# Kernel tuning notes

Measured on AMD Instinct MI355X. Metric: run time of the kernel, lower is better.

## Reference

```python
import jax, jax.numpy as jnp
import numpy as np
import math

B, L, D = 8, 2048, 768
ORDER, EMB = 128, 5
FFT = 2 * L
MIN_DECAY = math.log(0.01) / 1.5   # slow_decay_pct = 1.5
MAX_DECAY = math.log(0.01) / 0.3   # fast_decay_pct = 0.3
SHIFT = 0.0


def _pos_emb(seq_len, emb_dim):
    # pos_emb_init from the source: [t, Re(z), Im(z)] with bands = (emb_dim-1)//2
    bands = (emb_dim - 1) // 2
    t = jnp.linspace(0.0, 1.0, seq_len)[None, :, None]
    t_res = jnp.linspace(0.0, seq_len - 1, seq_len)[None, :, None]
    w = 2.0 * jnp.pi * t_res / seq_len
    f = jnp.linspace(1e-4, bands - 1, bands)[None, None]
    zc = jnp.exp(-1j * f * w)
    return jnp.concatenate([t, zc.real, zc.imag], axis=-1).astype(jnp.float32)  # (1, L, EMB)


def setup_inputs() -> dict:
    key = jax.random.key(0)
    ks = jax.random.split(key, 16)
    s = 0.02
    return {
        "u": jax.random.normal(ks[0], (B, L, D), jnp.float32),
        "in_W": jax.random.normal(ks[1], (D, 3 * D), jnp.float32) * s,
        "in_b": jnp.zeros((3 * D,), jnp.float32),
        "out_W": jax.random.normal(ks[2], (D, D), jnp.float32) * s,
        "out_b": jnp.zeros((D,), jnp.float32),
        "x1_s": jax.random.normal(ks[3], (D, 4), jnp.float32) * 0.25,
        "x2_s": jax.random.normal(ks[4], (D, 4), jnp.float32) * 0.25,
        "v_s": jax.random.normal(ks[5], (D, 4), jnp.float32) * 0.25,
        "x1_sb": jax.random.normal(ks[6], (D,), jnp.float32) * 0.1,
        "x2_sb": jax.random.normal(ks[7], (D,), jnp.float32) * 0.1,
        "v_sb": jax.random.normal(ks[8], (D,), jnp.float32) * 0.1,
        "D_bias": jax.random.normal(ks[9], (D,), jnp.float32),
        "z": _pos_emb(L, EMB),
        "sin_freq": 10.0 * jnp.ones((1, ORDER), jnp.float32),   # hyena_w = 10
        "eo_mat": jax.random.normal(ks[10], (1, EMB, ORDER), jnp.float32) * 0.3,
        "eo_bias": jnp.zeros((1, ORDER), jnp.float32),
        "oo1_mat": jax.random.normal(ks[11], (1, ORDER, ORDER), jnp.float32) * 0.08,
        "oo1_bias": jnp.zeros((1, ORDER), jnp.float32),
        "oo2_mat": jax.random.normal(ks[12], (1, ORDER, ORDER), jnp.float32) * 0.08,
        "oo2_bias": jnp.zeros((1, ORDER), jnp.float32),
        "oh_mat": jax.random.normal(ks[13], (1, ORDER, D), jnp.float32) * 0.08,
    }


def _depthwise4(x, w, b):
    # torch Conv1d(groups=3D, kernel=4, padding=3) truncated to [:L] == causal conv, left pad 3
    out = jax.lax.conv_general_dilated(
        x, w[:, None, :], window_strides=(1,), padding=[(3, 0)],
        dimension_numbers=("NCH", "OIH", "NCH"), feature_group_count=x.shape[1])
    return out + b[None, :, None]


def _hyena_filter(z, sin_freq, eo_mat, eo_bias, oo1_mat, oo1_bias, oo2_mat, oo2_bias, oh_mat):
    # then exponential decay modulation (exp_mod_in_place_fwd), channels=1, reverse=0.
    f = sin_freq[:, None, :]                                       # (1, 1, ORDER)
    h = jnp.sin(f * (jnp.einsum("cle,ceo->clo", z, eo_mat) + eo_bias[:, None, :]))
    h = jnp.sin(f * (jnp.einsum("clo,cop->clp", h, oo1_mat) + oo1_bias[:, None, :]))
    h = jnp.sin(f * (jnp.einsum("clo,cop->clp", h, oo2_mat) + oo2_bias[:, None, :]))
    k = jnp.einsum("clo,coh->clh", h, oh_mat)                      # (1, L, D)
    t = jnp.linspace(0.0, 1.0, k.shape[1])
    deltas = jnp.abs(jnp.linspace(MIN_DECAY, MAX_DECAY, k.shape[2]))
    k = k * (jnp.exp(-t[None, :, None] * deltas[None, None, :]) + SHIFT)
    return k[0].T                                                  # (D, L)


def _forward(u, in_W, in_b, out_W, out_b, x1_s, x2_s, v_s, x1_sb, x2_sb, v_sb,
             D_bias, z, sin_freq, eo_mat, eo_bias, oo1_mat, oo1_bias,
             oo2_mat, oo2_bias, oh_mat):
    seqlen = u.shape[1]
    k = _hyena_filter(z, sin_freq, eo_mat, eo_bias, oo1_mat, oo1_bias, oo2_mat, oo2_bias, oh_mat)
    x1x2v = u @ in_W + in_b                                        # (B, L, 3D)
    x1, x2, v = jnp.split(x1x2v, 3, axis=-1)
    x1 = jnp.transpose(x1, (0, 2, 1))                              # (B, D, L)
    x2 = jnp.transpose(x2, (0, 2, 1))
    v = jnp.transpose(v, (0, 2, 1))
    x1 = _depthwise4(x1, x1_s, x1_sb)
    x2 = _depthwise4(x2, x2_s, x2_sb)
    v = _depthwise4(v, v_s, v_sb)
    v = v * x1                                                     # first gate
    k_f = jnp.fft.rfft(k.astype(jnp.float32), n=FFT)               # (D, FFT//2+1)
    v_f = jnp.fft.rfft(v.astype(jnp.float32), n=FFT)               # (B, D, FFT//2+1)
    y = jnp.fft.irfft(v_f * k_f[None], n=FFT)[..., :seqlen]        # long FFT conv
    y = y + v * D_bias[None, :, None]                              # skip term
    y = y * x2                                                     # second gate
    y = jnp.transpose(y, (0, 2, 1))                                # (B, L, D)
    return y @ out_W + out_b


def reference(u, in_W, in_b, out_W, out_b, x1_s, x2_s, v_s, x1_sb, x2_sb, v_sb,
              D_bias, z, sin_freq, eo_mat, eo_bias, oo1_mat, oo1_bias,
              oo2_mat, oo2_bias, oh_mat):
    return _forward(u, in_W, in_b, out_W, out_b, x1_s, x2_s, v_s, x1_sb, x2_sb, v_sb,
                    D_bias, z, sin_freq, eo_mat, eo_bias, oo1_mat, oo1_bias,
                    oo2_mat, oo2_bias, oh_mat)
```

## Files before the change

kernel.cpp:

```cpp
#include <hip/hip_runtime.h>


typedef __bf16 bf16x8 __attribute__((ext_vector_type(8)));
typedef float  f32x4  __attribute__((ext_vector_type(4)));

#define AS1 __attribute__((address_space(1)))
#define AS3 __attribute__((address_space(3)))
#define GLD16(gp, lp) __builtin_amdgcn_global_load_lds((AS1 void*)(void*)(gp), (AS3 void*)(void*)(lp), 16, 0, 0)

#define LGKM_BAR       __asm__ __volatile__("s_waitcnt lgkmcnt(0)\n\ts_barrier" ::: "memory")
#define VM_LGKM_BAR(N) __asm__ __volatile__("s_waitcnt vmcnt(" #N ") lgkmcnt(0)\n\ts_barrier" ::: "memory")

__device__ __forceinline__ unsigned short f2b(float f) {
    unsigned u = __builtin_bit_cast(unsigned, f);
    unsigned r = (u + 0x7fffu + ((u >> 16) & 1u)) >> 16;
    return (unsigned short)r;
}
__device__ __forceinline__ float b2f_lo(unsigned u) {
    return __builtin_bit_cast(float, u << 16);
}
__device__ __forceinline__ float b2f_hi(unsigned u) {
    return __builtin_bit_cast(float, u & 0xffff0000u);
}

__device__ __forceinline__ float2 cmul(float2 a, float2 b) {
    return make_float2(a.x * b.x - a.y * b.y, a.x * b.y + a.y * b.x);
}
__device__ __forceinline__ float2 cadd(float2 a, float2 b) { return make_float2(a.x + b.x, a.y + b.y); }
__device__ __forceinline__ float2 csub(float2 a, float2 b) { return make_float2(a.x - b.x, a.y - b.y); }

#define TWO_PI 6.283185307179586f

#define BFLY(i,j)   { float2 ta=x[i], tb=x[j]; x[i]=cadd(ta,tb); x[j]=csub(ta,tb); }
#define BFLYW(i,j,w){ float2 ta=x[i], tb=x[j]; x[i]=cadd(ta,tb); x[j]=cmul(csub(ta,tb),(w)); }
#define BFLYI(i,j)  { float2 ta=x[i], tb=x[j]; x[i]=cadd(ta,tb); float2 tt=csub(ta,tb); x[j]=make_float2(-dd*tt.y, dd*tt.x); }
#define CSWAP(i,j)  { float2 tt=x[i]; x[i]=x[j]; x[j]=tt; }

template<int DIR, bool UZ>
__device__ __forceinline__ void dft16(float2* x) {
    const float dd = (float)DIR;
    const float C1 = 0.92387953251128674f, S1 = 0.38268343236508977f, R2 = 0.70710678118654752f;
    const float2 W1 = make_float2( C1, dd*S1);
    const float2 W2 = make_float2( R2, dd*R2);
    const float2 W3 = make_float2( S1, dd*C1);
    const float2 W5 = make_float2(-S1, dd*C1);
    const float2 W6 = make_float2(-R2, dd*R2);
    const float2 W7 = make_float2(-C1, dd*S1);
    if (UZ) {
        x[8]  = x[0];
        x[9]  = cmul(x[1], W1);
        x[10] = cmul(x[2], W2);
        x[11] = cmul(x[3], W3);
        x[12] = make_float2(-dd*x[4].y, dd*x[4].x);
        x[13] = cmul(x[5], W5);
        x[14] = cmul(x[6], W6);
        x[15] = cmul(x[7], W7);
    } else {
        BFLY(0,8); BFLYW(1,9,W1); BFLYW(2,10,W2); BFLYW(3,11,W3);
        BFLYI(4,12); BFLYW(5,13,W5); BFLYW(6,14,W6); BFLYW(7,15,W7);
    }
    BFLY(0,4);  BFLYW(1,5,W2);  BFLYI(2,6);   BFLYW(3,7,W6);
    BFLY(8,12); BFLYW(9,13,W2); BFLYI(10,14); BFLYW(11,15,W6);
    BFLY(0,2);  BFLYI(1,3);  BFLY(4,6);   BFLYI(5,7);
    BFLY(8,10); BFLYI(9,11); BFLY(12,14); BFLYI(13,15);
    BFLY(0,1); BFLY(2,3); BFLY(4,5); BFLY(6,7);
    BFLY(8,9); BFLY(10,11); BFLY(12,13); BFLY(14,15);
    CSWAP(1,8); CSWAP(2,4); CSWAP(3,12); CSWAP(5,10); CSWAP(7,14); CSWAP(11,13);
}

__device__ __forceinline__ void twiddle16(float2* x, float ang) {
    float s, c; __sincosf(ang, &s, &c);
    const float2 u1  = make_float2(c, s);
    const float2 u2  = cmul(u1, u1);
    const float2 u3  = cmul(u2, u1);
    const float2 u4  = cmul(u2, u2);
    const float2 u8  = cmul(u4, u4);
    const float2 u12 = cmul(u8, u4);
    x[1]  = cmul(x[1],  u1);
    x[2]  = cmul(x[2],  u2);
    x[3]  = cmul(x[3],  u3);
    x[4]  = cmul(x[4],  u4);
    x[5]  = cmul(x[5],  cmul(u4, u1));
    x[6]  = cmul(x[6],  cmul(u4, u2));
    x[7]  = cmul(x[7],  cmul(u4, u3));
    x[8]  = cmul(x[8],  u8);
    x[9]  = cmul(x[9],  cmul(u8, u1));
    x[10] = cmul(x[10], cmul(u8, u2));
    x[11] = cmul(x[11], cmul(u8, u3));
    x[12] = cmul(x[12], u12);
    x[13] = cmul(x[13], cmul(u12, u1));
    x[14] = cmul(x[14], cmul(u12, u2));
    x[15] = cmul(x[15], cmul(u12, u3));
}

__device__ __forceinline__ int ph1(int row, int col) { return row * 256 + (col ^ row); }
__device__ __forceinline__ int ph2(int row, int col) { return row * 16 + (col ^ (row & 15)); }

__device__ __forceinline__ void fft4096_fwd(float2* x, float2* lds, int t) {
    dft16<-1, true>(x);
    twiddle16(x, -(float)t * (TWO_PI / 4096.0f));
    #pragma unroll
    for (int k1 = 0; k1 < 16; ++k1) lds[ph1(k1, t)] = x[k1];
    __syncthreads();
    const int hi = t >> 4, lo = t & 15;
    #pragma unroll
    for (int t1 = 0; t1 < 16; ++t1) x[t1] = lds[ph1(hi, t1 * 16 + lo)];
    dft16<-1, false>(x);
    twiddle16(x, -(float)lo * (TWO_PI / 256.0f));
    __syncthreads();
    #pragma unroll
    for (int k2 = 0; k2 < 16; ++k2) lds[ph2(t, k2)] = x[k2];
    __syncthreads();
    #pragma unroll
    for (int t0 = 0; t0 < 16; ++t0) x[t0] = lds[ph2(hi * 16 + t0, lo)];
    dft16<-1, false>(x);
}

__device__ __forceinline__ void fft4096_inv(float2* x, float2* lds, int t) {
    const int hi = t >> 4, lo = t & 15;
    dft16<1, false>(x);
    __syncthreads();
    #pragma unroll
    for (int t0 = 0; t0 < 16; ++t0) lds[ph2(hi * 16 + t0, lo)] = x[t0];
    __syncthreads();
    #pragma unroll
    for (int k2 = 0; k2 < 16; ++k2) x[k2] = lds[ph2(t, k2)];
    twiddle16(x, (float)lo * (TWO_PI / 256.0f));
    dft16<1, false>(x);
    __syncthreads();
    #pragma unroll
    for (int t1 = 0; t1 < 16; ++t1) lds[ph1(hi, t1 * 16 + lo)] = x[t1];
    __syncthreads();
    #pragma unroll
    for (int k1 = 0; k1 < 16; ++k1) x[k1] = lds[ph1(k1, t)];
    twiddle16(x, (float)t * (TWO_PI / 4096.0f));
    dft16<1, false>(x);
}

__global__ __launch_bounds__(256) void filter_k_kernel(
    const float* __restrict__ z, const float* __restrict__ sf,
    const float* __restrict__ eo, const float* __restrict__ eo_b,
    const float* __restrict__ oo1, const float* __restrict__ oo1_b,
    const float* __restrict__ oo2, const float* __restrict__ oo2_b,
    const float* __restrict__ oh, float* __restrict__ kfil)
{
    __shared__ float h3buf[4][128];
    __shared__ float htmp[2][128];
    const int t = threadIdx.x;
    const int l0 = blockIdx.x * 4;
    const int half = t >> 7;
    const int o = t & 127;
    const float sfo = sf[o];
    for (int p = 0; p < 2; ++p) {
        const int li = p * 2 + half;
        const int l = l0 + li;
        float a = eo_b[o];
        #pragma unroll
        for (int e = 0; e < 5; ++e) a += z[l * 5 + e] * eo[e * 128 + o];
        htmp[half][o] = sinf(sfo * a);
        __syncthreads();
        float a2 = oo1_b[o];
        for (int q = 0; q < 128; ++q) a2 += htmp[half][q] * oo1[q * 128 + o];
        const float h2 = sinf(sfo * a2);
        __syncthreads();
        htmp[half][o] = h2;
        __syncthreads();
        float a3 = oo2_b[o];
        for (int q = 0; q < 128; ++q) a3 += htmp[half][q] * oo2[q * 128 + o];
        h3buf[li][o] = sinf(sfo * a3);
        __syncthreads();
    }
    const float MIND = -3.070113457325394f;
    const float MAXD = -15.350567286626972f;
    for (int c = 0; c < 3; ++c) {
        const int h = t + c * 256;
        float acc[4];
        #pragma unroll
        for (int li = 0; li < 4; ++li) acc[li] = 0.f;
        for (int q = 0; q < 128; ++q) {
            const float w = oh[q * 768 + h];
            #pragma unroll
            for (int li = 0; li < 4; ++li) acc[li] += h3buf[li][q] * w;
        }
        const float delta = fabsf(MIND + (MAXD - MIND) * (float)h * (1.0f / 767.0f));
        #pragma unroll
        for (int li = 0; li < 4; ++li) {
            const int l = l0 + li;
            const float tt = (float)l * (1.0f / 2047.0f);
            kfil[h * 2048 + l] = acc[li] * expf(-tt * delta);
        }
    }
}

__global__ __launch_bounds__(256) void filter_fft_kernel(
    const float* __restrict__ kfil, const float* __restrict__ D_bias,
    float2* __restrict__ Kf)
{
    __shared__ __align__(16) float2 lds[4096];
    const int d = blockIdx.x, t = threadIdx.x;
    float2 x[16];
    #pragma unroll
    for (int r = 0; r < 8; ++r) x[r] = make_float2(kfil[d * 2048 + r * 256 + t], 0.f);
    fft4096_fwd(x, lds, t);
    const float db = D_bias[d];
    const float s = 1.0f / 4096.0f;
    #pragma unroll
    for (int k3 = 0; k3 < 16; ++k3)
        Kf[d * 4096 + k3 * 256 + t] = make_float2((x[k3].x + db) * s, x[k3].y * s);
}

__global__ __launch_bounds__(256) void convert_u_kernel(
    const float* __restrict__ u, unsigned short* __restrict__ ub)
{
    const int g = blockIdx.x * 256 + threadIdx.x;
    const float4 v = ((const float4*)u)[g];
    uint2 o;
    o.x = (unsigned)f2b(v.x) | ((unsigned)f2b(v.y) << 16);
    o.y = (unsigned)f2b(v.z) | ((unsigned)f2b(v.w) << 16);
    ((uint2*)ub)[g] = o;
}

__global__ __launch_bounds__(256) void transpose_W_kernel(
    const float* __restrict__ W, unsigned short* __restrict__ Wt, int K, int N)
{
    __shared__ float tile[32][33];
    const int n0 = blockIdx.x * 32, k0 = blockIdx.y * 32;
    const int tx = threadIdx.x & 31, ty = threadIdx.x >> 5;
    #pragma unroll
    for (int r = 0; r < 4; ++r) {
        const int kk = ty + r * 8;
        tile[kk][tx] = W[(k0 + kk) * N + n0 + tx];
    }
    __syncthreads();
    #pragma unroll
    for (int r = 0; r < 4; ++r) {
        const int nn = ty + r * 8;
        Wt[(n0 + nn) * K + k0 + tx] = f2b(tile[tx][nn]);
    }
}

__global__ __launch_bounds__(256) void transpose_Y_kernel(
    const unsigned short* __restrict__ Y, unsigned short* __restrict__ Yt)
{
    __shared__ unsigned short tile[32][34];
    const int bx = blockIdx.x;
    const int l0 = (bx & 63) * 32;
    const int tmp = bx >> 6;
    const int d0 = (tmp % 24) * 32;
    const int b  = tmp / 24;
    const int tx = threadIdx.x & 31, ty = threadIdx.x >> 5;
    #pragma unroll
    for (int r = 0; r < 4; ++r) {
        const int dd = ty + r * 8;
        tile[dd][tx] = Y[(b * 768 + d0 + dd) * 2048 + l0 + tx];
    }
    __syncthreads();
    #pragma unroll
    for (int r = 0; r < 4; ++r) {
        const int ll = ty + r * 8;
        Yt[(b * 2048 + l0 + ll) * 768 + d0 + tx] = tile[tx][ll];
    }
}

__global__ __launch_bounds__(512, 2) void gemm256_kernel(
    const unsigned short* __restrict__ A,
    const unsigned short* __restrict__ Bm,
    const float* __restrict__ bias,
    unsigned short* __restrict__ outb,
    float* __restrict__ outf,
    int mode)
{
    extern __shared__ __align__(16) unsigned short lds[];
    unsigned short* As = lds;
    unsigned short* Bs = lds + 32768;
    const int t = threadIdx.x;
    const int wv = t >> 6, lane = t & 63;
    const int row0 = (mode == 0 ? blockIdx.y : blockIdx.x) * 256;
    const int col0 = (mode == 0 ? blockIdx.x : blockIdx.y) * 256;
    const int wr = wv >> 2, wc = wv & 3;
    const int frow = lane & 15, kc = lane >> 4;

    f32x4 acc[8][4] = {};

    const int srow = t >> 3;
    const int cdat = (t & 7) ^ (srow & 7);
    const unsigned short* gA = A  + (row0 + srow) * 768 + cdat * 8;
    const unsigned short* gB = Bm + (col0 + srow) * 768 + cdat * 8;

#define STG_A(buf, q, koff) GLD16(gA + (q) * 49152 + (koff), (char*)As + (buf) * 32768 + (q) * 8192 + wv * 1024)
#define STG_B(buf, q, koff) GLD16(gB + (q) * 49152 + (koff), (char*)Bs + (buf) * 32768 + (q) * 8192 + wv * 1024)

    const int sx = frow & 7;
    const int aRowBase = (wr * 128 + frow) * 64;
    const int bRowBase = (wc * 64 + frow) * 64;
    const int sl0 = ((0 + kc) ^ sx) * 8;
    const int sl1 = ((4 + kc) ^ sx) * 8;

    bf16x8 aF[4][2], bN0[2][2], bN1[2][2];

#define READ_A(buf, mh)                                                         \
    _Pragma("unroll") for (int m = 0; m < 4; ++m) {                             \
        aF[m][0] = *(const bf16x8*)(As + (buf) * 16384 + aRowBase + ((mh) * 4 + m) * 1024 + sl0); \
        aF[m][1] = *(const bf16x8*)(As + (buf) * 16384 + aRowBase + ((mh) * 4 + m) * 1024 + sl1); \
    }
#define READ_B(buf, nh, arr)                                                    \
    _Pragma("unroll") for (int n = 0; n < 2; ++n) {                             \
        arr[n][0] = *(const bf16x8*)(Bs + (buf) * 16384 + bRowBase + ((nh) * 2 + n) * 1024 + sl0); \
        arr[n][1] = *(const bf16x8*)(Bs + (buf) * 16384 + bRowBase + ((nh) * 2 + n) * 1024 + sl1); \
    }
#define MFMA_Q(mh, nh, arr)                                                     \
    __builtin_amdgcn_s_setprio(1);                                              \
    _Pragma("unroll") for (int m = 0; m < 4; ++m)                               \
    _Pragma("unroll") for (int n = 0; n < 2; ++n)                               \
    _Pragma("unroll") for (int ks = 0; ks < 2; ++ks)                            \
        acc[(mh) * 4 + m][(nh) * 2 + n] = __builtin_amdgcn_mfma_f32_16x16x32_bf16( \
            aF[m][ks], arr[n][ks], acc[(mh) * 4 + m][(nh) * 2 + n], 0, 0, 0);   \
    __builtin_amdgcn_s_setprio(0);

    STG_A(0, 0, 0); STG_A(0, 1, 0); STG_A(0, 2, 0); STG_A(0, 3, 0);
    STG_B(0, 0, 0); STG_B(0, 1, 0); STG_B(0, 2, 0); STG_B(0, 3, 0);
    STG_A(1, 0, 64); STG_A(1, 2, 64);
    STG_B(1, 0, 64); STG_B(1, 1, 64); STG_B(1, 2, 64); STG_B(1, 3, 64);
    VM_LGKM_BAR(6);

    for (int i = 0; i < 5; ++i) {
        const int k1 = (2 * i + 1) * 64, k2 = (2 * i + 2) * 64, k3 = (2 * i + 3) * 64;
        READ_A(0, 0); READ_B(0, 0, bN0);
        STG_A(1, 1, k1); STG_A(1, 3, k1);
        MFMA_Q(0, 0, bN0);
        LGKM_BAR;
        READ_B(0, 1, bN1);
        STG_A(0, 0, k2); STG_A(0, 2, k2);
        MFMA_Q(0, 1, bN1);
        LGKM_BAR;
        READ_A(0, 1);
        STG_B(0, 0, k2); STG_B(0, 1, k2);
        MFMA_Q(1, 1, bN1);
        LGKM_BAR;
        STG_B(0, 2, k2); STG_B(0, 3, k2);
        MFMA_Q(1, 0, bN0);
        VM_LGKM_BAR(6);
        READ_A(1, 0); READ_B(1, 0, bN0);
        STG_A(0, 1, k2); STG_A(0, 3, k2);
        MFMA_Q(0, 0, bN0);
        LGKM_BAR;
        READ_B(1, 1, bN1);
        STG_A(1, 0, k3); STG_A(1, 2, k3);
        MFMA_Q(0, 1, bN1);
        LGKM_BAR;
        READ_A(1, 1);
        STG_B(1, 0, k3); STG_B(1, 1, k3);
        MFMA_Q(1, 1, bN1);
        LGKM_BAR;
        STG_B(1, 2, k3); STG_B(1, 3, k3);
        MFMA_Q(1, 0, bN0);
        VM_LGKM_BAR(6);
    }

    {
        READ_A(0, 0); READ_B(0, 0, bN0);
        STG_A(1, 1, 704); STG_A(1, 3, 704);
        MFMA_Q(0, 0, bN0);
        LGKM_BAR;
        READ_B(0, 1, bN1);
        MFMA_Q(0, 1, bN1);
        LGKM_BAR;
        READ_A(0, 1);
        MFMA_Q(1, 1, bN1);
        LGKM_BAR;
        MFMA_Q(1, 0, bN0);
        VM_LGKM_BAR(2);
        READ_A(1, 0); READ_B(1, 0, bN0);
        MFMA_Q(0, 0, bN0);
        LGKM_BAR;
        READ_B(1, 1, bN1);
        MFMA_Q(0, 1, bN1);
        VM_LGKM_BAR(0);
        READ_A(1, 1);
        MFMA_Q(1, 1, bN1);
        MFMA_Q(1, 0, bN0);
    }
#undef READ_A
#undef READ_B
#undef MFMA_Q
#undef STG_A
#undef STG_B

    if (mode == 0) {
        const int part = row0 / 768;
        const int bb = col0 / 2048;
        unsigned short* Xp = outb + (size_t)(part * 8 + bb) * 768 * 2048;
        const int drow0 = row0 - part * 768 + wr * 128 + (lane >> 4) * 4;
        const int lcol0 = col0 - bb * 2048 + wc * 64 + frow;
        #pragma unroll
        for (int m = 0; m < 8; ++m) {
            #pragma unroll
            for (int rr = 0; rr < 4; ++rr) {
                const int dd = drow0 + m * 16 + rr;
                const float bn = bias[row0 + wr * 128 + (lane >> 4) * 4 + m * 16 + rr];
                #pragma unroll
                for (int n = 0; n < 4; ++n)
                    Xp[dd * 2048 + lcol0 + n * 16] = f2b(acc[m][n][rr] + bn);
            }
        }
    } else {
        #pragma unroll
        for (int m = 0; m < 8; ++m) {
            #pragma unroll
            for (int rr = 0; rr < 4; ++rr) {
                const int mm = row0 + wr * 128 + (lane >> 4) * 4 + m * 16 + rr;
                #pragma unroll
                for (int n = 0; n < 4; ++n) {
                    const int nn = col0 + wc * 64 + n * 16 + frow;
                    outf[(size_t)mm * 768 + nn] = acc[m][n][rr] + bias[nn];
                }
            }
        }
    }
}

__device__ __forceinline__ void conv6(const unsigned short* __restrict__ p,
                                      const float* w, float bias, int t, float* out8)
{
    const uint4 m = *(const uint4*)(p + 8 * t);
    uint2 q = make_uint2(0u, 0u);
    if (t) q = *(const uint2*)(p + 8 * t - 4);
    float s[12];
    s[0] = b2f_lo(q.x); s[1] = b2f_hi(q.x); s[2] = b2f_lo(q.y); s[3] = b2f_hi(q.y);
    s[4] = b2f_lo(m.x); s[5] = b2f_hi(m.x); s[6] = b2f_lo(m.y); s[7] = b2f_hi(m.y);
    s[8] = b2f_lo(m.z); s[9] = b2f_hi(m.z); s[10] = b2f_lo(m.w); s[11] = b2f_hi(m.w);
    #pragma unroll
    for (int i = 0; i < 8; ++i)
        out8[i] = bias + w[0] * s[i + 1] + w[1] * s[i + 2] + w[2] * s[i + 3] + w[3] * s[i + 4];
}

__global__ __launch_bounds__(256) void fft_conv_kernel(
    const unsigned short* __restrict__ X, const float2* __restrict__ Kf,
    const float* __restrict__ x1_s, const float* __restrict__ x2_s, const float* __restrict__ v_s,
    const float* __restrict__ x1_sb, const float* __restrict__ x2_sb, const float* __restrict__ v_sb,
    unsigned short* __restrict__ Y)
{
    __shared__ __align__(16) float2 lds[4096];
    unsigned* ldsu = (unsigned*)lds;
    const int d = blockIdx.x, jp = blockIdx.y, t = threadIdx.x;
    const int b0 = jp * 2, b1 = b0 + 1;

    const unsigned short* px1a = X + ((size_t)(0 * 8 + b0) * 768 + d) * 2048;
    const unsigned short* pva  = X + ((size_t)(2 * 8 + b0) * 768 + d) * 2048;
    const unsigned short* px1b = X + ((size_t)(0 * 8 + b1) * 768 + d) * 2048;
    const unsigned short* pvb  = X + ((size_t)(2 * 8 + b1) * 768 + d) * 2048;

    {
        float w1[4], wv[4];
        #pragma unroll
        for (int j = 0; j < 4; ++j) { w1[j] = x1_s[d * 4 + j]; wv[j] = v_s[d * 4 + j]; }
        const float bc1 = x1_sb[d], bcv = v_sb[d];
        float pa[8];
        {
            float va[8], g[8];
            conv6(pva,  wv, bcv, t, va);
            conv6(px1a, w1, bc1, t, g);
            #pragma unroll
            for (int i = 0; i < 8; ++i) pa[i] = va[i] * g[i];
        }
        {
            float vb[8], g[8];
            conv6(pvb,  wv, bcv, t, vb);
            conv6(px1b, w1, bc1, t, g);
            unsigned vh[8];
            #pragma unroll
            for (int i = 0; i < 8; ++i)
                vh[i] = (unsigned)f2b(pa[i]) | ((unsigned)f2b(vb[i] * g[i]) << 16);
            *(uint4*)(ldsu + 8 * t)     = make_uint4(vh[0], vh[1], vh[2], vh[3]);
            *(uint4*)(ldsu + 8 * t + 4) = make_uint4(vh[4], vh[5], vh[6], vh[7]);
        }
    }
    __syncthreads();

    float2 x[16];
    #pragma unroll
    for (int r = 0; r < 8; ++r) {
        const unsigned u = ldsu[r * 256 + t];
        x[r] = make_float2(b2f_lo(u), b2f_hi(u));
    }
    __syncthreads();

    fft4096_fwd(x, lds, t);

    {
        const float2* kf = Kf + (size_t)d * 4096;
        #pragma unroll
        for (int c4 = 0; c4 < 4; ++c4) {
            float2 kr[4];
            #pragma unroll
            for (int j = 0; j < 4; ++j) kr[j] = kf[(c4 * 4 + j) * 256 + t];
            #pragma unroll
            for (int j = 0; j < 4; ++j) x[c4 * 4 + j] = cmul(x[c4 * 4 + j], kr[j]);
            __asm__ __volatile__("" ::: "memory");
        }
    }

    fft4096_inv(x, lds, t);

    __syncthreads();
    {
        const unsigned short* px2a = X + ((size_t)(1 * 8 + b0) * 768 + d) * 2048;
        const unsigned short* px2b = X + ((size_t)(1 * 8 + b1) * 768 + d) * 2048;
        float w2[4];
        #pragma unroll
        for (int j = 0; j < 4; ++j) w2[j] = x2_s[d * 4 + j];
        const float bc2 = x2_sb[d];
        float ga[8], gb[8];
        conv6(px2a, w2, bc2, t, ga);
        conv6(px2b, w2, bc2, t, gb);
        unsigned c2[8];
        #pragma unroll
        for (int i = 0; i < 8; ++i)
            c2[i] = (unsigned)f2b(ga[i]) | ((unsigned)f2b(gb[i]) << 16);
        *(uint4*)(ldsu + 8 * t)     = make_uint4(c2[0], c2[1], c2[2], c2[3]);
        *(uint4*)(ldsu + 8 * t + 4) = make_uint4(c2[4], c2[5], c2[6], c2[7]);
    }
    __syncthreads();

    unsigned short* ya = Y + ((size_t)b0 * 768 + d) * 2048;
    unsigned short* yb = Y + ((size_t)b1 * 768 + d) * 2048;
    #pragma unroll
    for (int n1 = 0; n1 < 8; ++n1) {
        const int l = n1 * 256 + t;
        const unsigned u = ldsu[l];
        ya[l] = f2b(x[n1].x * b2f_lo(u));
        yb[l] = f2b(x[n1].y * b2f_hi(u));
    }
}

extern "C" void kernel_launch(void* const* d_in, const int* in_sizes, int n_in,
                              void* d_out, int out_size, void* d_ws, size_t ws_size,
                              hipStream_t stream)
{
    (void)in_sizes; (void)n_in; (void)out_size; (void)ws_size;
    const float* u      = (const float*)d_in[0];
    const float* in_W   = (const float*)d_in[1];
    const float* in_b   = (const float*)d_in[2];
    const float* out_W  = (const float*)d_in[3];
    const float* out_b  = (const float*)d_in[4];
    const float* x1_s   = (const float*)d_in[5];
    const float* x2_s   = (const float*)d_in[6];
    const float* v_s    = (const float*)d_in[7];
    const float* x1_sb  = (const float*)d_in[8];
    const float* x2_sb  = (const float*)d_in[9];
    const float* v_sb   = (const float*)d_in[10];
    const float* D_bias = (const float*)d_in[11];
    const float* z      = (const float*)d_in[12];
    const float* sf     = (const float*)d_in[13];
    const float* eo     = (const float*)d_in[14];
    const float* eo_b   = (const float*)d_in[15];
    const float* oo1    = (const float*)d_in[16];
    const float* oo1_b  = (const float*)d_in[17];
    const float* oo2    = (const float*)d_in[18];
    const float* oo2_b  = (const float*)d_in[19];
    const float* oh     = (const float*)d_in[20];
    float* out = (float*)d_out;

    char* ws = (char*)d_ws;
    unsigned short* Xbf  = (unsigned short*)(ws + 0);
    unsigned short* Ybf  = (unsigned short*)(ws + 75497472);
    unsigned short* ubYt = (unsigned short*)(ws + 100663296);
    unsigned short* Wt   = (unsigned short*)(ws + 125829120);
    unsigned short* W2t  = (unsigned short*)(ws + 129368064);
    float*          kfil = (float*)(ws + 130547712);
    float2*         Kf   = (float2*)(ws + 136839168);

    static int attr_set = 0;
    if (!attr_set) {
        (void)hipFuncSetAttribute(reinterpret_cast<const void*>(gemm256_kernel),
                                  hipFuncAttributeMaxDynamicSharedMemorySize, 131072);
        attr_set = 1;
    }

    filter_k_kernel<<<512, 256, 0, stream>>>(z, sf, eo, eo_b, oo1, oo1_b, oo2, oo2_b, oh, kfil);
    filter_fft_kernel<<<768, 256, 0, stream>>>(kfil, D_bias, Kf);
    convert_u_kernel<<<12288, 256, 0, stream>>>(u, ubYt);
    transpose_W_kernel<<<dim3(72, 24), 256, 0, stream>>>(in_W, Wt, 768, 2304);
    transpose_W_kernel<<<dim3(24, 24), 256, 0, stream>>>(out_W, W2t, 768, 768);
    gemm256_kernel<<<dim3(64, 9), 512, 131072, stream>>>(Wt, ubYt, in_b, Xbf, nullptr, 0);
    fft_conv_kernel<<<dim3(768, 4), 256, 0, stream>>>(Xbf, Kf, x1_s, x2_s, v_s, x1_sb, x2_sb, v_sb, Ybf);
    transpose_Y_kernel<<<12288, 256, 0, stream>>>(Ybf, ubYt);
    gemm256_kernel<<<dim3(64, 3), 512, 131072, stream>>>(ubYt, W2t, out_b, nullptr, out, 1);
}
```

Before: 361.6 us.

## Template GEMM with 192x256 tiles and simpler two-phase double-buffered pipeline

Replaces the hand-scheduled 256x256 GEMM with a templated kernel that uses 192x256 (input projection) and 256x192 (output projection) tiles. The grids grow to 768 and 256 blocks, which fills the CUs more evenly with less tail waste. The fine-grained interleaved staging is replaced by a simple two-buffer pipeline: it stages one k-tile while computing the other, with a full vmcnt(0) barrier per tile. This simpler schedule may expose more load latency than the previous interleaved one.

Result: faster. 348.2 us (-3.7%).

```diff
diff --git a/kernel.cpp b/kernel.cpp
--- a/kernel.cpp
+++ b/kernel.cpp
@@ -262,156 +262,113 @@
     }
 }
 
-__global__ __launch_bounds__(512, 2) void gemm256_kernel(
+template<int TM, int TN, int WR, int WC, int MODE>
+__global__ __launch_bounds__(512, 2) void gemm2ph_kernel(
     const unsigned short* __restrict__ A,
     const unsigned short* __restrict__ Bm,
     const float* __restrict__ bias,
     unsigned short* __restrict__ outb,
-    float* __restrict__ outf,
-    int mode)
-{
+    float* __restrict__ outf)
+{
+    constexpr int MF = TM / WR / 16;
+    constexpr int NF = TN / WC / 16;
+    constexpr int QA = TM / 64;
+    constexpr int QB = TN / 64;
     extern __shared__ __align__(16) unsigned short lds[];
     unsigned short* As = lds;
-    unsigned short* Bs = lds + 32768;
+    unsigned short* Bs = lds + 2 * TM * 64;
     const int t = threadIdx.x;
     const int wv = t >> 6, lane = t & 63;
-    const int row0 = (mode == 0 ? blockIdx.y : blockIdx.x) * 256;
-    const int col0 = (mode == 0 ? blockIdx.x : blockIdx.y) * 256;
-    const int wr = wv >> 2, wc = wv & 3;
+    const int row0 = (MODE == 0 ? blockIdx.y : blockIdx.x) * TM;
+    const int col0 = (MODE == 0 ? blockIdx.x : blockIdx.y) * TN;
+    const int wr = wv / WC, wc = wv % WC;
     const int frow = lane & 15, kc = lane >> 4;
 
-    f32x4 acc[8][4] = {};
+    f32x4 acc[MF][NF] = {};
 
     const int srow = t >> 3;
     const int cdat = (t & 7) ^ (srow & 7);
     const unsigned short* gA = A  + (row0 + srow) * 768 + cdat * 8;
     const unsigned short* gB = Bm + (col0 + srow) * 768 + cdat * 8;
 
-#define STG_A(buf, q, koff) GLD16(gA + (q) * 49152 + (koff), (char*)As + (buf) * 32768 + (q) * 8192 + wv * 1024)
-#define STG_B(buf, q, koff) GLD16(gB + (q) * 49152 + (koff), (char*)Bs + (buf) * 32768 + (q) * 8192 + wv * 1024)
-
-    const int sx = frow & 7;
-    const int aRowBase = (wr * 128 + frow) * 64;
-    const int bRowBase = (wc * 64 + frow) * 64;
-    const int sl0 = ((0 + kc) ^ sx) * 8;
-    const int sl1 = ((4 + kc) ^ sx) * 8;
-
-    bf16x8 aF[4][2], bN0[2][2], bN1[2][2];
-
-#define READ_A(buf, mh)                                                         \
-    _Pragma("unroll") for (int m = 0; m < 4; ++m) {                             \
-        aF[m][0] = *(const bf16x8*)(As + (buf) * 16384 + aRowBase + ((mh) * 4 + m) * 1024 + sl0); \
-        aF[m][1] = *(const bf16x8*)(As + (buf) * 16384 + aRowBase + ((mh) * 4 + m) * 1024 + sl1); \
-    }
-#define READ_B(buf, nh, arr)                                                    \
-    _Pragma("unroll") for (int n = 0; n < 2; ++n) {                             \
-        arr[n][0] = *(const bf16x8*)(Bs + (buf) * 16384 + bRowBase + ((nh) * 2 + n) * 1024 + sl0); \
-        arr[n][1] = *(const bf16x8*)(Bs + (buf) * 16384 + bRowBase + ((nh) * 2 + n) * 1024 + sl1); \
-    }
-#define MFMA_Q(mh, nh, arr)                                                     \
-    __builtin_amdgcn_s_setprio(1);                                              \
-    _Pragma("unroll") for (int m = 0; m < 4; ++m)                               \
-    _Pragma("unroll") for (int n = 0; n < 2; ++n)                               \
-    _Pragma("unroll") for (int ks = 0; ks < 2; ++ks)                            \
-        acc[(mh) * 4 + m][(nh) * 2 + n] = __builtin_amdgcn_mfma_f32_16x16x32_bf16( \
-            aF[m][ks], arr[n][ks], acc[(mh) * 4 + m][(nh) * 2 + n], 0, 0, 0);   \
-    __builtin_amdgcn_s_setprio(0);
-
-    STG_A(0, 0, 0); STG_A(0, 1, 0); STG_A(0, 2, 0); STG_A(0, 3, 0);
-    STG_B(0, 0, 0); STG_B(0, 1, 0); STG_B(0, 2, 0); STG_B(0, 3, 0);
-    STG_A(1, 0, 64); STG_A(1, 2, 64);
-    STG_B(1, 0, 64); STG_B(1, 1, 64); STG_B(1, 2, 64); STG_B(1, 3, 64);
-    VM_LGKM_BAR(6);
-
-    for (int i = 0; i < 5; ++i) {
-        const int k1 = (2 * i + 1) * 64, k2 = (2 * i + 2) * 64, k3 = (2 * i + 3) * 64;
-        READ_A(0, 0); READ_B(0, 0, bN0);
-        STG_A(1, 1, k1); STG_A(1, 3, k1);
-        MFMA_Q(0, 0, bN0);
-        LGKM_BAR;
-        READ_B(0, 1, bN1);
-        STG_A(0, 0, k2); STG_A(0, 2, k2);
-        MFMA_Q(0, 1, bN1);
-        LGKM_BAR;
-        READ_A(0, 1);
-        STG_B(0, 0, k2); STG_B(0, 1, k2);
-        MFMA_Q(1, 1, bN1);
-        LGKM_BAR;
-        STG_B(0, 2, k2); STG_B(0, 3, k2);
-        MFMA_Q(1, 0, bN0);
-        VM_LGKM_BAR(6);
-        READ_A(1, 0); READ_B(1, 0, bN0);
-        STG_A(0, 1, k2); STG_A(0, 3, k2);
-        MFMA_Q(0, 0, bN0);
-        LGKM_BAR;
-        READ_B(1, 1, bN1);
-        STG_A(1, 0, k3); STG_A(1, 2, k3);
-        MFMA_Q(0, 1, bN1);
-        LGKM_BAR;
-        READ_A(1, 1);
-        STG_B(1, 0, k3); STG_B(1, 1, k3);
-        MFMA_Q(1, 1, bN1);
-        LGKM_BAR;
-        STG_B(1, 2, k3); STG_B(1, 3, k3);
-        MFMA_Q(1, 0, bN0);
-        VM_LGKM_BAR(6);
-    }
-
-    {
-        READ_A(0, 0); READ_B(0, 0, bN0);
-        STG_A(1, 1, 704); STG_A(1, 3, 704);
-        MFMA_Q(0, 0, bN0);
-        LGKM_BAR;
-        READ_B(0, 1, bN1);
-        MFMA_Q(0, 1, bN1);
-        LGKM_BAR;
-        READ_A(0, 1);
-        MFMA_Q(1, 1, bN1);
-        LGKM_BAR;
-        MFMA_Q(1, 0, bN0);
-        VM_LGKM_BAR(2);
-        READ_A(1, 0); READ_B(1, 0, bN0);
-        MFMA_Q(0, 0, bN0);
-        LGKM_BAR;
-        READ_B(1, 1, bN1);
-        MFMA_Q(0, 1, bN1);
+#define STAGE(buf, kt)                                                        \
+    {                                                                         \
+        _Pragma("unroll") for (int q = 0; q < QA; ++q)                        \
+            GLD16(gA + q * 49152 + (kt) * 64,                                 \
+                  (char*)As + (buf) * (TM * 128) + q * 8192 + wv * 1024);     \
+        _Pragma("unroll") for (int q = 0; q < QB; ++q)                        \
+            GLD16(gB + q * 49152 + (kt) * 64,                                 \
+                  (char*)Bs + (buf) * (TN * 128) + q * 8192 + wv * 1024);     \
+    }
+
+#define HALF(buf, ks)                                                         \
+    {                                                                         \
+        bf16x8 aF[MF], bF[NF];                                                \
+        _Pragma("unroll") for (int m = 0; m < MF; ++m) {                      \
+            const int r = wr * (TM / WR) + m * 16 + frow;                     \
+            aF[m] = *(const bf16x8*)(As + (buf) * (TM * 64) + r * 64 +        \
+                                     ((((ks) * 4 + kc) ^ (r & 7)) << 3));     \
+        }                                                                     \
+        _Pragma("unroll") for (int n = 0; n < NF; ++n) {                      \
+            const int r = wc * (TN / WC) + n * 16 + frow;                     \
+            bF[n] = *(const bf16x8*)(Bs + (buf) * (TN * 64) + r * 64 +        \
+                                     ((((ks) * 4 + kc) ^ (r & 7)) << 3));     \
+        }                                                                     \
+        __builtin_amdgcn_s_setprio(1);                                        \
+        _Pragma("unroll") for (int m = 0; m < MF; ++m)                        \
+        _Pragma("unroll") for (int n = 0; n < NF; ++n)                        \
+            acc[m][n] = __builtin_amdgcn_mfma_f32_16x16x32_bf16(              \
+                aF[m], bF[n], acc[m][n], 0, 0, 0);                            \
+        __builtin_amdgcn_s_setprio(0);                                        \
+    }
+
+    STAGE(0, 0);
+    STAGE(1, 1);
+    VM_LGKM_BAR(7);
+
+    HALF(0, 0); HALF(0, 1);
+    VM_LGKM_BAR(0);
+
+    #pragma unroll 1
+    for (int kt = 1; kt <= 9; kt += 2) {
+        STAGE(0, kt + 1);
+        HALF(1, 0); HALF(1, 1);
         VM_LGKM_BAR(0);
-        READ_A(1, 1);
-        MFMA_Q(1, 1, bN1);
-        MFMA_Q(1, 0, bN0);
-    }
-#undef READ_A
-#undef READ_B
-#undef MFMA_Q
-#undef STG_A
-#undef STG_B
-
-    if (mode == 0) {
+        STAGE(1, kt + 2);
+        HALF(0, 0); HALF(0, 1);
+        VM_LGKM_BAR(0);
+    }
+
+    HALF(1, 0); HALF(1, 1);
+#undef STAGE
+#undef HALF
+
+    if (MODE == 0) {
         const int part = row0 / 768;
         const int bb = col0 / 2048;
         unsigned short* Xp = outb + (size_t)(part * 8 + bb) * 768 * 2048;
-        const int drow0 = row0 - part * 768 + wr * 128 + (lane >> 4) * 4;
-        const int lcol0 = col0 - bb * 2048 + wc * 64 + frow;
-        #pragma unroll
-        for (int m = 0; m < 8; ++m) {
+        const int drow0 = row0 - part * 768 + wr * (TM / WR) + kc * 4;
+        const int lcol0 = col0 - bb * 2048 + wc * (TN / WC) + frow;
+        #pragma unroll
+        for (int m = 0; m < MF; ++m) {
             #pragma unroll
             for (int rr = 0; rr < 4; ++rr) {
                 const int dd = drow0 + m * 16 + rr;
-                const float bn = bias[row0 + wr * 128 + (lane >> 4) * 4 + m * 16 + rr];
+                const float bn = bias[row0 + wr * (TM / WR) + kc * 4 + m * 16 + rr];
                 #pragma unroll
-                for (int n = 0; n < 4; ++n)
+                for (int n = 0; n < NF; ++n)
                     Xp[dd * 2048 + lcol0 + n * 16] = f2b(acc[m][n][rr] + bn);
             }
         }
     } else {
         #pragma unroll
-        for (int m = 0; m < 8; ++m) {
+        for (int m = 0; m < MF; ++m) {
             #pragma unroll
             for (int rr = 0; rr < 4; ++rr) {
-                const int mm = row0 + wr * 128 + (lane >> 4) * 4 + m * 16 + rr;
+                const int mm = row0 + wr * (TM / WR) + kc * 4 + m * 16 + rr;
                 #pragma unroll
-                for (int n = 0; n < 4; ++n) {
-                    const int nn = col0 + wc * 64 + n * 16 + frow;
+                for (int n = 0; n < NF; ++n) {
+                    const int nn = col0 + wc * (TN / WC) + n * 16 + frow;
                     outf[(size_t)mm * 768 + nn] = acc[m][n][rr] + bias[nn];
                 }
             }
@@ -572,8 +529,12 @@
 
     static int attr_set = 0;
     if (!attr_set) {
-        (void)hipFuncSetAttribute(reinterpret_cast<const void*>(gemm256_kernel),
-                                  hipFuncAttributeMaxDynamicSharedMemorySize, 131072);
+        (void)hipFuncSetAttribute(
+            reinterpret_cast<const void*>(&gemm2ph_kernel<192, 256, 2, 4, 0>),
+            hipFuncAttributeMaxDynamicSharedMemorySize, 114688);
+        (void)hipFuncSetAttribute(
+            reinterpret_cast<const void*>(&gemm2ph_kernel<256, 192, 4, 2, 1>),
+            hipFuncAttributeMaxDynamicSharedMemorySize, 114688);
         attr_set = 1;
     }
 
@@ -582,8 +543,10 @@
     convert_u_kernel<<<12288, 256, 0, stream>>>(u, ubYt);
     transpose_W_kernel<<<dim3(72, 24), 256, 0, stream>>>(in_W, Wt, 768, 2304);
     transpose_W_kernel<<<dim3(24, 24), 256, 0, stream>>>(out_W, W2t, 768, 768);
-    gemm256_kernel<<<dim3(64, 9), 512, 131072, stream>>>(Wt, ubYt, in_b, Xbf, nullptr, 0);
+    gemm2ph_kernel<192, 256, 2, 4, 0><<<dim3(64, 12), 512, 114688, stream>>>(
+        Wt, ubYt, in_b, Xbf, nullptr);
     fft_conv_kernel<<<dim3(768, 4), 256, 0, stream>>>(Xbf, Kf, x1_s, x2_s, v_s, x1_sb, x2_sb, v_sb, Ybf);
     transpose_Y_kernel<<<12288, 256, 0, stream>>>(Ybf, ubYt);
-    gemm256_kernel<<<dim3(64, 3), 512, 131072, stream>>>(ubYt, W2t, out_b, nullptr, out, 1);
-}
+    gemm2ph_kernel<256, 192, 4, 2, 1><<<dim3(64, 4), 512, 114688, stream>>>(
+        ubYt, W2t, out_b, nullptr, out);
+}
```
